# Kernel optimization log

Hardware: AMD Instinct MI355X
Metric: run time of the kernel (lower is better)

Reference implementation:

```python
import jax, jax.numpy as jnp
import numpy as np

B, L, D, H = 2, 1024, 1024, 16
Dh = D // H


def setup_inputs() -> dict:
    key = jax.random.key(0)
    ks = jax.random.split(key, 11)
    w_scale = 1.0 / np.sqrt(D).astype(np.float32)
    def w(k):
        return jax.random.normal(k, (D, D), dtype=jnp.float32) * w_scale
    def b(k):
        return jax.random.normal(k, (D,), dtype=jnp.float32) * 0.01
    return {
        "x": jax.random.normal(ks[0], (B, L, D), dtype=jnp.float32),
        "Wq": w(ks[1]), "bq": b(ks[2]),
        "Wk1": w(ks[3]), "bk1": b(ks[4]),
        "Wv": w(ks[5]), "bv": b(ks[6]),
        "Wk2": w(ks[7]), "bk2": b(ks[8]),
        "Wp": w(ks[9]), "bp": b(ks[10]),
    }


def reference(x, Wq, bq, Wk1, bk1, Wv, bv, Wk2, bk2, Wp, bp):
    Bx, Lx, Dx = x.shape
    lin = lambda t, W, b_: t @ W + b_
    # AR branch: kernelized accumulation of K^T V
    Q = lin(x, Wq, bq).reshape(Bx, Lx, H, Dh)      # (B,L,H,Dh)
    K = lin(x, Wk1, bk1).reshape(Bx, Lx, H, Dh)
    V = lin(x, Wv, bv).reshape(Bx, Lx, H, Dh)
    Wacc = jnp.cumsum(jnp.einsum('blhd,blhe->blhde', K, V), axis=1)  # (B,L,H,Dh,Dh)
    O1 = jnp.einsum('blhd,blhde->blhe', Q, Wacc)   # (B,L,H,Dh)
    # MA branch on one-step residuals
    V_raw = x.reshape(Bx, Lx, H, Dh)
    E = V_raw[:, 1:] - O1[:, :-1]                  # (B,L-1,H,Dh)
    z = lin(x[:, :-1], Wk2, bk2) / jnp.sqrt(jnp.float32(Dx))
    k2 = jax.nn.sigmoid(z * 0.02).reshape(Bx, Lx - 1, H, Dh)
    q2 = -jax.nn.leaky_relu(-Q[:, :-1] / jnp.sqrt(jnp.float32(Dh)), negative_slope=0.02)
    WE = jnp.cumsum(jnp.einsum('blhd,blhe->blhde', k2, E), axis=1)  # (B,L-1,H,Dh,Dh)
    O2 = jnp.einsum('blhd,blhde->blhe', q2, WE)
    O2 = jnp.concatenate([jnp.zeros_like(O2[:, :1]), O2], axis=1)   # (B,L,H,Dh)
    y = (O1 + O2).reshape(Bx, Lx, Dx)
    return lin(y, Wp, bp)
```

## Files before the change

kernel.cpp:

```cpp
#include <hip/hip_runtime.h>
#include <hip/hip_bf16.h>
#include <math.h>

#define Bsz 2
#define Lsz 1024
#define Dsz 1024
#define Hsz 16
#define Dh 64
#define Mtot (Bsz*Lsz)
#define NC (Lsz/64)
#define LPAD 72

typedef __bf16 bf16_t;
typedef bf16_t bf16x8 __attribute__((ext_vector_type(8)));
typedef bf16_t bf16x4 __attribute__((ext_vector_type(4)));
typedef float f32x4v __attribute__((ext_vector_type(4)));

__device__ __forceinline__ void gload16(const void* g, void* l) {
    __builtin_amdgcn_global_load_lds(
        (const __attribute__((address_space(1))) unsigned int*)g,
        (__attribute__((address_space(3))) unsigned int*)l, 16, 0, 0);
}

template<int MODE>
__global__ __launch_bounds__(256) void bgemm_kernel(
    const bf16_t* __restrict__ A, const bf16_t* __restrict__ Bt,
    const float* b0, const float* b1, const float* b2, const float* b3,
    bf16_t* Qo, bf16_t* q2o, bf16_t* Ko, bf16_t* Vo, bf16_t* k2o, float* Cout)
{
    __shared__ __align__(16) bf16_t As[3][4096];
    __shared__ __align__(16) bf16_t Bs[3][4096];
    const int tid  = threadIdx.x;
    const int lane = tid & 63;
    const int wid  = tid >> 6;

    const int lin = blockIdx.x;
    const int xcd = lin & 7;
    const int t0  = lin >> 3;
    int brow, bcolg;
    if (MODE == 0) {
        brow  = (xcd & 1) * 8 + (t0 & 7);
        bcolg = (xcd >> 1) * 8 + (t0 >> 3);
    } else {
        brow  = (xcd & 3) * 4 + (t0 & 3);
        bcolg = (xcd >> 2) * 4 + (t0 >> 2);
    }
    const int row0  = brow * 128;
    const int col0g = bcolg * 128;
    const int p    = col0g >> 10;
    const int col0 = col0g & 1023;
    const int wr = (wid >> 1) * 64;
    const int wc = (wid & 1) * 64;

    const int srow = tid >> 2;
    const int scol = tid & 3;
    const int ssw  = (srow & 3) ^ ((srow >> 2) & 3);
    const int scol_sw = scol ^ ssw;
    const bf16_t* gA0 = A  + (size_t)(row0 + srow)       * 1024 + scol_sw * 8;
    const bf16_t* gA1 = A  + (size_t)(row0 + srow + 64)  * 1024 + scol_sw * 8;
    const bf16_t* gB0 = Bt + (size_t)(col0g + srow)      * 1024 + scol_sw * 8;
    const bf16_t* gB1 = Bt + (size_t)(col0g + srow + 64) * 1024 + scol_sw * 8;

    const int laneRow = lane & 15;
    const int kblk = lane >> 4;
    const int swz = (kblk ^ (laneRow & 3) ^ ((laneRow >> 2) & 3)) & 3;
    const int aoff = (wr + laneRow) * 32 + swz * 8;
    const int boff = (wc + laneRow) * 32 + swz * 8;

    f32x4v acc[4][4];
    #pragma unroll
    for (int i = 0; i < 4; ++i)
        #pragma unroll
        for (int j = 0; j < 4; ++j)
            acc[i][j] = (f32x4v){0.f, 0.f, 0.f, 0.f};

    auto stage = [&](int buf) {
        gload16(gA0, &As[buf][tid * 8]);
        gload16(gA1, &As[buf][(tid + 256) * 8]);
        gload16(gB0, &Bs[buf][tid * 8]);
        gload16(gB1, &Bs[buf][(tid + 256) * 8]);
        gA0 += 32; gA1 += 32; gB0 += 32; gB1 += 32;
    };

    stage(0); stage(1); stage(2);
    asm volatile("s_waitcnt vmcnt(8)" ::: "memory");
    __builtin_amdgcn_s_barrier();

    int cur = 0;
    for (int t = 0; t < 32; ++t) {
        bf16x8 af[4], bfr[4];
        #pragma unroll
        for (int f = 0; f < 4; ++f) {
            af[f]  = *reinterpret_cast<const bf16x8*>(&As[cur][aoff + f * 512]);
            bfr[f] = *reinterpret_cast<const bf16x8*>(&Bs[cur][boff + f * 512]);
        }
        asm volatile("s_waitcnt lgkmcnt(0)" ::: "memory");
        __builtin_amdgcn_s_barrier();
        if (t < 29) stage(cur);
        #pragma unroll
        for (int i = 0; i < 4; ++i)
            #pragma unroll
            for (int j = 0; j < 4; ++j)
                acc[i][j] = __builtin_amdgcn_mfma_f32_16x16x32_bf16(af[i], bfr[j], acc[i][j], 0, 0, 0);
        if (t < 29)      { asm volatile("s_waitcnt vmcnt(8)" ::: "memory"); }
        else if (t == 29){ asm volatile("s_waitcnt vmcnt(4)" ::: "memory"); }
        else             { asm volatile("s_waitcnt vmcnt(0)" ::: "memory"); }
        __builtin_amdgcn_s_barrier();
        cur = (cur == 2) ? 0 : cur + 1;
    }

    const int crowb = row0 + wr + kblk * 4;
    const int ccolb = col0 + wc + laneRow;
    const float* bias = (MODE == 1) ? b0 : (p == 0) ? b0 : (p == 1) ? b1 : (p == 2) ? b2 : b3;
    float bv[4];
    #pragma unroll
    for (int j = 0; j < 4; ++j) bv[j] = bias[ccolb + j * 16];
    #pragma unroll
    for (int i = 0; i < 4; ++i)
        #pragma unroll
        for (int j = 0; j < 4; ++j)
            #pragma unroll
            for (int e = 0; e < 4; ++e) {
                const float val = acc[i][j][e] + bv[j];
                const size_t idx = (size_t)(crowb + i * 16 + e) * 1024 + ccolb + j * 16;
                if (MODE == 1) {
                    Cout[idx] = val;
                } else if (p == 0) {
                    Qo[idx]  = (bf16_t)val;
                    q2o[idx] = (bf16_t)((val >= 0.f ? 0.02f * val : val) * 0.125f);
                } else if (p == 1) {
                    Ko[idx] = (bf16_t)val;
                } else if (p == 2) {
                    Vo[idx] = (bf16_t)val;
                } else {
                    k2o[idx] = (bf16_t)(1.f / (1.f + __expf(-val * 0.000625f)));
                }
            }
}

__global__ __launch_bounds__(256) void prep_kernel(
    const float* __restrict__ x, bf16_t* __restrict__ xb,
    const float* __restrict__ W0, const float* __restrict__ W1,
    const float* __restrict__ W2, const float* __restrict__ W3,
    const float* __restrict__ W4, bf16_t* __restrict__ Wt)
{
    const int z = blockIdx.z;
    const int tid = threadIdx.x;
    if (z == 5) {
        const int lin = blockIdx.y * 16 + blockIdx.x;
        #pragma unroll
        for (int u = 0; u < 8; ++u) {
            const size_t s = (size_t)lin * 2048 + u * 256 + tid;
            float4 v = *reinterpret_cast<const float4*>(&x[s * 4]);
            bf16x4 o;
            o[0] = (bf16_t)v.x; o[1] = (bf16_t)v.y; o[2] = (bf16_t)v.z; o[3] = (bf16_t)v.w;
            *reinterpret_cast<bf16x4*>(&xb[s * 4]) = o;
        }
        return;
    }
    const float* W = (z == 0) ? W0 : (z == 1) ? W1 : (z == 2) ? W2 : (z == 3) ? W3 : W4;
    bf16_t* T = Wt + (size_t)z * 1048576;

    __shared__ float Ls[64][65];
    const int k0 = blockIdx.x * 64;
    const int n0 = blockIdx.y * 64;
    const int r  = tid >> 4;
    const int c4 = (tid & 15) * 4;
    #pragma unroll
    for (int i = 0; i < 4; ++i) {
        float4 v = *reinterpret_cast<const float4*>(&W[(size_t)(k0 + r + i * 16) * Dsz + n0 + c4]);
        Ls[r + i * 16][c4 + 0] = v.x;
        Ls[r + i * 16][c4 + 1] = v.y;
        Ls[r + i * 16][c4 + 2] = v.z;
        Ls[r + i * 16][c4 + 3] = v.w;
    }
    __syncthreads();
    #pragma unroll
    for (int i = 0; i < 4; ++i) {
        const int n = r + i * 16;
        bf16x4 o;
        o[0] = (bf16_t)Ls[c4 + 0][n];
        o[1] = (bf16_t)Ls[c4 + 1][n];
        o[2] = (bf16_t)Ls[c4 + 2][n];
        o[3] = (bf16_t)Ls[c4 + 3][n];
        *reinterpret_cast<bf16x4*>(&T[(size_t)(n0 + n) * Dsz + k0 + c4]) = o;
    }
}

__global__ __launch_bounds__(256) void chunk_intra_kernel(
    const bf16_t* __restrict__ Ap, const bf16_t* __restrict__ Kp,
    const bf16_t* __restrict__ Vp, float* __restrict__ Oi, bf16_t* __restrict__ dT)
{
    __shared__ __align__(16) bf16_t sQ[64 * LPAD];
    __shared__ __align__(16) bf16_t sK[64 * LPAD];
    __shared__ __align__(16) bf16_t sKt[64 * LPAD];
    __shared__ __align__(16) bf16_t sVt[64 * LPAD];
    __shared__ __align__(16) bf16_t sP[64 * LPAD];

    const int bid = blockIdx.x;
    const int c  = bid & (NC - 1);
    const int bh = bid >> 4;
    const int b = bh >> 4, h = bh & 15;
    const int tid = threadIdx.x;
    const size_t gbase = ((size_t)b * Lsz + (size_t)c * 64) * Dsz + h * Dh;

    #pragma unroll
    for (int cc = tid; cc < 512; cc += 256) {
        const int j = cc >> 3;
        const int d0 = (cc & 7) * 8;
        const size_t g = gbase + (size_t)j * 1024 + d0;
        bf16x8 qv = *reinterpret_cast<const bf16x8*>(&Ap[g]);
        bf16x8 kv = *reinterpret_cast<const bf16x8*>(&Kp[g]);
        bf16x8 vv = *reinterpret_cast<const bf16x8*>(&Vp[g]);
        *reinterpret_cast<bf16x8*>(&sQ[j * LPAD + d0]) = qv;
        *reinterpret_cast<bf16x8*>(&sK[j * LPAD + d0]) = kv;
        #pragma unroll
        for (int i = 0; i < 8; ++i) {
            sKt[(d0 + i) * LPAD + j] = kv[i];
            sVt[(d0 + i) * LPAD + j] = vv[i];
        }
    }
    __syncthreads();

    const int w = tid >> 6;
    const int lane = tid & 63;
    const int lr = lane & 15;
    const int kb = lane >> 4;
    const int m0 = w * 16;

    f32x4v accp[4];
    #pragma unroll
    for (int n = 0; n < 4; ++n) accp[n] = (f32x4v){0.f, 0.f, 0.f, 0.f};
    #pragma unroll
    for (int kk = 0; kk < 2; ++kk) {
        bf16x8 a = *reinterpret_cast<const bf16x8*>(&sQ[(m0 + lr) * LPAD + kk * 32 + kb * 8]);
        #pragma unroll
        for (int n = 0; n < 4; ++n) {
            bf16x8 bb = *reinterpret_cast<const bf16x8*>(&sK[(n * 16 + lr) * LPAD + kk * 32 + kb * 8]);
            accp[n] = __builtin_amdgcn_mfma_f32_16x16x32_bf16(a, bb, accp[n], 0, 0, 0);
        }
    }
    f32x4v acct[4];
    #pragma unroll
    for (int n = 0; n < 4; ++n) acct[n] = (f32x4v){0.f, 0.f, 0.f, 0.f};
    #pragma unroll
    for (int kk = 0; kk < 2; ++kk) {
        bf16x8 a = *reinterpret_cast<const bf16x8*>(&sVt[(m0 + lr) * LPAD + kk * 32 + kb * 8]);
        #pragma unroll
        for (int n = 0; n < 4; ++n) {
            bf16x8 bb = *reinterpret_cast<const bf16x8*>(&sKt[(n * 16 + lr) * LPAD + kk * 32 + kb * 8]);
            acct[n] = __builtin_amdgcn_mfma_f32_16x16x32_bf16(a, bb, acct[n], 0, 0, 0);
        }
    }

    const size_t tbase = (size_t)bid * 4096;
    #pragma unroll
    for (int n = 0; n < 4; ++n)
        #pragma unroll
        for (int e = 0; e < 4; ++e) {
            const int r = m0 + kb * 4 + e;
            const int col = n * 16 + lr;
            dT[tbase + (size_t)r * 64 + col] = (bf16_t)acct[n][e];
            float pv = (col <= r) ? accp[n][e] : 0.f;
            sP[r * LPAD + col] = (bf16_t)pv;
        }
    __syncthreads();

    f32x4v acco[4];
    #pragma unroll
    for (int n = 0; n < 4; ++n) acco[n] = (f32x4v){0.f, 0.f, 0.f, 0.f};
    #pragma unroll
    for (int kk = 0; kk < 2; ++kk) {
        bf16x8 a = *reinterpret_cast<const bf16x8*>(&sP[(m0 + lr) * LPAD + kk * 32 + kb * 8]);
        #pragma unroll
        for (int n = 0; n < 4; ++n) {
            bf16x8 bb = *reinterpret_cast<const bf16x8*>(&sVt[(n * 16 + lr) * LPAD + kk * 32 + kb * 8]);
            acco[n] = __builtin_amdgcn_mfma_f32_16x16x32_bf16(a, bb, acco[n], 0, 0, 0);
        }
    }
    #pragma unroll
    for (int n = 0; n < 4; ++n)
        #pragma unroll
        for (int e = 0; e < 4; ++e)
            Oi[gbase + (size_t)(m0 + kb * 4 + e) * 1024 + n * 16 + lr] = acco[n][e];
}

__global__ __launch_bounds__(256) void chunk_prefix_kernel(bf16_t* dT)
{
    const int g = blockIdx.x;
    const int bh = g >> 4;
    const int slice = g & 15;
    bf16_t* base = dT + (size_t)bh * NC * 4096 + slice * 256 + threadIdx.x;
    float acc = 0.f;
    #pragma unroll
    for (int c = 0; c < NC; ++c) {
        float v = (float)base[(size_t)c * 4096];
        base[(size_t)c * 4096] = (bf16_t)acc;
        acc += v;
    }
}

template<int BR>
__global__ __launch_bounds__(256) void chunk_inter_kernel(
    const bf16_t* __restrict__ Ap, const bf16_t* __restrict__ T,
    const float* __restrict__ Oi, const float* __restrict__ xin,
    float* __restrict__ O1out, bf16_t* __restrict__ ebout)
{
    __shared__ __align__(16) bf16_t sA[64 * LPAD];
    __shared__ __align__(16) bf16_t sT[64 * LPAD];

    const int bid = blockIdx.x;
    const int c  = bid & (NC - 1);
    const int bh = bid >> 4;
    const int b = bh >> 4, h = bh & 15;
    const int tid = threadIdx.x;
    const size_t gbase = ((size_t)b * Lsz + (size_t)c * 64) * Dsz + h * Dh;

    #pragma unroll
    for (int cc = tid; cc < 512; cc += 256) {
        const int j = cc >> 3;
        const int d0 = (cc & 7) * 8;
        bf16x8 av = *reinterpret_cast<const bf16x8*>(&Ap[gbase + (size_t)j * 1024 + d0]);
        *reinterpret_cast<bf16x8*>(&sA[j * LPAD + d0]) = av;
    }
    {
        const size_t tb = (size_t)bid * 4096;
        const int row = tid >> 2;
        const int c16 = (tid & 3) * 16;
        bf16x8 v0 = *reinterpret_cast<const bf16x8*>(&T[tb + (size_t)row * 64 + c16]);
        bf16x8 v1 = *reinterpret_cast<const bf16x8*>(&T[tb + (size_t)row * 64 + c16 + 8]);
        *reinterpret_cast<bf16x8*>(&sT[row * LPAD + c16]) = v0;
        *reinterpret_cast<bf16x8*>(&sT[row * LPAD + c16 + 8]) = v1;
    }
    __syncthreads();

    const int w = tid >> 6;
    const int lane = tid & 63;
    const int lr = lane & 15;
    const int kb = lane >> 4;
    const int m0 = w * 16;

    f32x4v acc[4];
    #pragma unroll
    for (int n = 0; n < 4; ++n) acc[n] = (f32x4v){0.f, 0.f, 0.f, 0.f};
    #pragma unroll
    for (int kk = 0; kk < 2; ++kk) {
        bf16x8 a = *reinterpret_cast<const bf16x8*>(&sA[(m0 + lr) * LPAD + kk * 32 + kb * 8]);
        #pragma unroll
        for (int n = 0; n < 4; ++n) {
            bf16x8 bb = *reinterpret_cast<const bf16x8*>(&sT[(n * 16 + lr) * LPAD + kk * 32 + kb * 8]);
            acc[n] = __builtin_amdgcn_mfma_f32_16x16x32_bf16(a, bb, acc[n], 0, 0, 0);
        }
    }

    #pragma unroll
    for (int n = 0; n < 4; ++n)
        #pragma unroll
        for (int e = 0; e < 4; ++e) {
            const int iLoc = m0 + kb * 4 + e;
            const int lglob = c * 64 + iLoc;
            const size_t idx = gbase + (size_t)iLoc * 1024 + n * 16 + lr;
            const float val = acc[n][e] + Oi[idx];
            if (BR == 1) {
                O1out[idx] = val;
                float ev = 0.f;
                if (lglob < Lsz - 1) ev = xin[idx + 1024] - val;
                ebout[idx] = (bf16_t)ev;
            } else {
                if (lglob < Lsz - 1) ebout[idx + 1024] = (bf16_t)(xin[idx + 1024] + val);
                if (lglob == 0)      ebout[idx] = (bf16_t)(xin[idx]);
            }
        }
}

extern "C" void kernel_launch(void* const* d_in, const int* in_sizes, int n_in,
                              void* d_out, int out_size, void* d_ws, size_t ws_size,
                              hipStream_t stream) {
    const float* x   = (const float*)d_in[0];
    const float* Wq  = (const float*)d_in[1];
    const float* bq  = (const float*)d_in[2];
    const float* Wk1 = (const float*)d_in[3];
    const float* bk1 = (const float*)d_in[4];
    const float* Wv  = (const float*)d_in[5];
    const float* bv  = (const float*)d_in[6];
    const float* Wk2 = (const float*)d_in[7];
    const float* bk2 = (const float*)d_in[8];
    const float* Wp  = (const float*)d_in[9];
    const float* bp  = (const float*)d_in[10];
    float* out = (float*)d_out;
    float* ws  = (float*)d_ws;

    const size_t mat = (size_t)Mtot * Dsz;
    float*  O1  = ws;
    float*  Oib = ws + mat;
    bf16_t* dT  = (bf16_t*)(ws + 2 * mat);
    bf16_t* xb  = (bf16_t*)(ws + 2 * mat + mat / 2);
    bf16_t* Wt  = (bf16_t*)(ws + 3 * mat);
    float*  b16base = ws + 3 * mat + 3 * mat;
    bf16_t* Qr  = (bf16_t*)(b16base);
    bf16_t* q2  = (bf16_t*)(b16base + mat / 2);
    bf16_t* Kb  = (bf16_t*)(b16base + 2 * (mat / 2));
    bf16_t* Vb  = (bf16_t*)(b16base + 3 * (mat / 2));
    bf16_t* k2  = (bf16_t*)(b16base + 4 * (mat / 2));
    bf16_t* Eb  = (bf16_t*)(b16base + 5 * (mat / 2));
    bf16_t* yb  = (bf16_t*)(b16base + 6 * (mat / 2));

    dim3 block(256);

    prep_kernel<<<dim3(16, 16, 6), block, 0, stream>>>(x, xb, Wq, Wk1, Wv, Wk2, Wp, Wt);

    bgemm_kernel<0><<<dim3(512), block, 0, stream>>>(
        xb, Wt, bq, bk1, bv, bk2, Qr, q2, Kb, Vb, k2, nullptr);

    chunk_intra_kernel<<<dim3(512), block, 0, stream>>>(Qr, Kb, Vb, Oib, dT);
    chunk_prefix_kernel<<<dim3(512), block, 0, stream>>>(dT);
    chunk_inter_kernel<1><<<dim3(512), block, 0, stream>>>(Qr, dT, Oib, x, O1, Eb);
    chunk_intra_kernel<<<dim3(512), block, 0, stream>>>(q2, k2, Eb, Oib, dT);
    chunk_prefix_kernel<<<dim3(512), block, 0, stream>>>(dT);
    chunk_inter_kernel<2><<<dim3(512), block, 0, stream>>>(q2, dT, Oib, O1, nullptr, yb);

    bgemm_kernel<1><<<dim3(128), block, 0, stream>>>(
        yb, Wt + 4 * 1048576, bp, nullptr, nullptr, nullptr,
        nullptr, nullptr, nullptr, nullptr, nullptr, out);
}
```

Measured before the change: 101.7 us.

## Fuse chunk prefix sum into inter kernel, 4-stage GEMM pipeline, bf16 intra output

```diff
diff --git a/kernel.cpp b/kernel.cpp
--- a/kernel.cpp
+++ b/kernel.cpp
@@ -28,8 +28,8 @@
     const float* b0, const float* b1, const float* b2, const float* b3,
     bf16_t* Qo, bf16_t* q2o, bf16_t* Ko, bf16_t* Vo, bf16_t* k2o, float* Cout)
 {
-    __shared__ __align__(16) bf16_t As[3][4096];
-    __shared__ __align__(16) bf16_t Bs[3][4096];
+    __shared__ __align__(16) bf16_t As[4][4096];
+    __shared__ __align__(16) bf16_t Bs[4][4096];
     const int tid  = threadIdx.x;
     const int lane = tid & 63;
     const int wid  = tid >> 6;
@@ -86,17 +86,15 @@
     asm volatile("s_waitcnt vmcnt(8)" ::: "memory");
     __builtin_amdgcn_s_barrier();
 
-    int cur = 0;
     for (int t = 0; t < 32; ++t) {
+        const int cur = t & 3;
         bf16x8 af[4], bfr[4];
         #pragma unroll
         for (int f = 0; f < 4; ++f) {
             af[f]  = *reinterpret_cast<const bf16x8*>(&As[cur][aoff + f * 512]);
             bfr[f] = *reinterpret_cast<const bf16x8*>(&Bs[cur][boff + f * 512]);
         }
-        asm volatile("s_waitcnt lgkmcnt(0)" ::: "memory");
-        __builtin_amdgcn_s_barrier();
-        if (t < 29) stage(cur);
+        if (t < 29) stage((t + 3) & 3);
         #pragma unroll
         for (int i = 0; i < 4; ++i)
             #pragma unroll
@@ -104,9 +102,8 @@
                 acc[i][j] = __builtin_amdgcn_mfma_f32_16x16x32_bf16(af[i], bfr[j], acc[i][j], 0, 0, 0);
         if (t < 29)      { asm volatile("s_waitcnt vmcnt(8)" ::: "memory"); }
         else if (t == 29){ asm volatile("s_waitcnt vmcnt(4)" ::: "memory"); }
-        else             { asm volatile("s_waitcnt vmcnt(0)" ::: "memory"); }
-        __builtin_amdgcn_s_barrier();
-        cur = (cur == 2) ? 0 : cur + 1;
+        else if (t == 30){ asm volatile("s_waitcnt vmcnt(0)" ::: "memory"); }
+        if (t < 31) __builtin_amdgcn_s_barrier();
     }
 
     const int crowb = row0 + wr + kblk * 4;
@@ -189,7 +186,7 @@
 
 __global__ __launch_bounds__(256) void chunk_intra_kernel(
     const bf16_t* __restrict__ Ap, const bf16_t* __restrict__ Kp,
-    const bf16_t* __restrict__ Vp, float* __restrict__ Oi, bf16_t* __restrict__ dT)
+    const bf16_t* __restrict__ Vp, bf16_t* __restrict__ Oi, bf16_t* __restrict__ dT)
 {
     __shared__ __align__(16) bf16_t sQ[64 * LPAD];
     __shared__ __align__(16) bf16_t sK[64 * LPAD];
@@ -282,29 +279,15 @@
     for (int n = 0; n < 4; ++n)
         #pragma unroll
         for (int e = 0; e < 4; ++e)
-            Oi[gbase + (size_t)(m0 + kb * 4 + e) * 1024 + n * 16 + lr] = acco[n][e];
-}
-
-__global__ __launch_bounds__(256) void chunk_prefix_kernel(bf16_t* dT)
-{
-    const int g = blockIdx.x;
-    const int bh = g >> 4;
-    const int slice = g & 15;
-    bf16_t* base = dT + (size_t)bh * NC * 4096 + slice * 256 + threadIdx.x;
-    float acc = 0.f;
-    #pragma unroll
-    for (int c = 0; c < NC; ++c) {
-        float v = (float)base[(size_t)c * 4096];
-        base[(size_t)c * 4096] = (bf16_t)acc;
-        acc += v;
-    }
+            Oi[gbase + (size_t)(m0 + kb * 4 + e) * 1024 + n * 16 + lr] = (bf16_t)acco[n][e];
 }
 
 template<int BR>
 __global__ __launch_bounds__(256) void chunk_inter_kernel(
-    const bf16_t* __restrict__ Ap, const bf16_t* __restrict__ T,
-    const float* __restrict__ Oi, const float* __restrict__ xin,
-    float* __restrict__ O1out, bf16_t* __restrict__ ebout)
+    const bf16_t* __restrict__ Ap, const bf16_t* __restrict__ dT,
+    const bf16_t* __restrict__ Oi, const float* __restrict__ xin,
+    const float* __restrict__ o1in, float* __restrict__ O1out,
+    bf16_t* __restrict__ ebout)
 {
     __shared__ __align__(16) bf16_t sA[64 * LPAD];
     __shared__ __align__(16) bf16_t sT[64 * LPAD];
@@ -324,13 +307,23 @@
         *reinterpret_cast<bf16x8*>(&sA[j * LPAD + d0]) = av;
     }
     {
-        const size_t tb = (size_t)bid * 4096;
+        const bf16_t* tb = dT + (size_t)bh * NC * 4096 + tid * 16;
+        float acc[16];
+        #pragma unroll
+        for (int k = 0; k < 16; ++k) acc[k] = 0.f;
+        for (int cc = 0; cc < c; ++cc) {
+            bf16x8 v0 = *reinterpret_cast<const bf16x8*>(&tb[(size_t)cc * 4096]);
+            bf16x8 v1 = *reinterpret_cast<const bf16x8*>(&tb[(size_t)cc * 4096 + 8]);
+            #pragma unroll
+            for (int k = 0; k < 8; ++k) { acc[k] += (float)v0[k]; acc[8 + k] += (float)v1[k]; }
+        }
         const int row = tid >> 2;
         const int c16 = (tid & 3) * 16;
-        bf16x8 v0 = *reinterpret_cast<const bf16x8*>(&T[tb + (size_t)row * 64 + c16]);
-        bf16x8 v1 = *reinterpret_cast<const bf16x8*>(&T[tb + (size_t)row * 64 + c16 + 8]);
-        *reinterpret_cast<bf16x8*>(&sT[row * LPAD + c16]) = v0;
-        *reinterpret_cast<bf16x8*>(&sT[row * LPAD + c16 + 8]) = v1;
+        bf16x8 o0, o1v;
+        #pragma unroll
+        for (int k = 0; k < 8; ++k) { o0[k] = (bf16_t)acc[k]; o1v[k] = (bf16_t)acc[8 + k]; }
+        *reinterpret_cast<bf16x8*>(&sT[row * LPAD + c16]) = o0;
+        *reinterpret_cast<bf16x8*>(&sT[row * LPAD + c16 + 8]) = o1v;
     }
     __syncthreads();
 
@@ -360,15 +353,15 @@
             const int iLoc = m0 + kb * 4 + e;
             const int lglob = c * 64 + iLoc;
             const size_t idx = gbase + (size_t)iLoc * 1024 + n * 16 + lr;
-            const float val = acc[n][e] + Oi[idx];
+            const float val = acc[n][e] + (float)Oi[idx];
             if (BR == 1) {
                 O1out[idx] = val;
                 float ev = 0.f;
                 if (lglob < Lsz - 1) ev = xin[idx + 1024] - val;
                 ebout[idx] = (bf16_t)ev;
             } else {
-                if (lglob < Lsz - 1) ebout[idx + 1024] = (bf16_t)(xin[idx + 1024] + val);
-                if (lglob == 0)      ebout[idx] = (bf16_t)(xin[idx]);
+                if (lglob < Lsz - 1) ebout[idx + 1024] = (bf16_t)(o1in[idx + 1024] + val);
+                if (lglob == 0)      ebout[idx] = (bf16_t)(o1in[idx]);
             }
         }
 }
@@ -392,18 +385,18 @@
 
     const size_t mat = (size_t)Mtot * Dsz;
     float*  O1  = ws;
-    float*  Oib = ws + mat;
-    bf16_t* dT  = (bf16_t*)(ws + 2 * mat);
-    bf16_t* xb  = (bf16_t*)(ws + 2 * mat + mat / 2);
-    bf16_t* Wt  = (bf16_t*)(ws + 3 * mat);
-    float*  b16base = ws + 3 * mat + 3 * mat;
-    bf16_t* Qr  = (bf16_t*)(b16base);
-    bf16_t* q2  = (bf16_t*)(b16base + mat / 2);
-    bf16_t* Kb  = (bf16_t*)(b16base + 2 * (mat / 2));
-    bf16_t* Vb  = (bf16_t*)(b16base + 3 * (mat / 2));
-    bf16_t* k2  = (bf16_t*)(b16base + 4 * (mat / 2));
-    bf16_t* Eb  = (bf16_t*)(b16base + 5 * (mat / 2));
-    bf16_t* yb  = (bf16_t*)(b16base + 6 * (mat / 2));
+    bf16_t* Oib = (bf16_t*)(ws + 2 * mat);
+    bf16_t* dT  = (bf16_t*)(ws + 3 * mat);
+    bf16_t* xb  = (bf16_t*)(ws + 4 * mat);
+    bf16_t* Wt  = (bf16_t*)(ws + 5 * mat);
+    float*  bb  = ws + 7 * mat + mat / 2;
+    bf16_t* Qr  = (bf16_t*)(bb);
+    bf16_t* q2  = (bf16_t*)(bb + mat / 2);
+    bf16_t* Kb  = (bf16_t*)(bb + mat);
+    bf16_t* Vb  = (bf16_t*)(bb + 3 * mat / 2);
+    bf16_t* k2  = (bf16_t*)(bb + 2 * mat);
+    bf16_t* Eb  = (bf16_t*)(bb + 5 * mat / 2);
+    bf16_t* yb  = Qr;
 
     dim3 block(256);
 
@@ -413,11 +406,9 @@
         xb, Wt, bq, bk1, bv, bk2, Qr, q2, Kb, Vb, k2, nullptr);
 
     chunk_intra_kernel<<<dim3(512), block, 0, stream>>>(Qr, Kb, Vb, Oib, dT);
-    chunk_prefix_kernel<<<dim3(512), block, 0, stream>>>(dT);
-    chunk_inter_kernel<1><<<dim3(512), block, 0, stream>>>(Qr, dT, Oib, x, O1, Eb);
+    chunk_inter_kernel<1><<<dim3(512), block, 0, stream>>>(Qr, dT, Oib, x, nullptr, O1, Eb);
     chunk_intra_kernel<<<dim3(512), block, 0, stream>>>(q2, k2, Eb, Oib, dT);
-    chunk_prefix_kernel<<<dim3(512), block, 0, stream>>>(dT);
-    chunk_inter_kernel<2><<<dim3(512), block, 0, stream>>>(q2, dT, Oib, O1, nullptr, yb);
+    chunk_inter_kernel<2><<<dim3(512), block, 0, stream>>>(q2, dT, Oib, nullptr, O1, nullptr, yb);
 
     bgemm_kernel<1><<<dim3(128), block, 0, stream>>>(
         yb, Wt + 4 * 1048576, bp, nullptr, nullptr, nullptr,
```

After: 100.7 us. Within noise of the previous version (-1.0%).
